# Optimization experiments

Measured on AMD Instinct MI355X. Metric: run time of the kernel, lower is better.

Reference implementation:

```python
import jax, jax.numpy as jnp
import numpy as np

K = 27          # kernel_size^3
N_IN = 150000   # active input sites
N_OUT = 150000  # active output sites
C_IN = 64
C_OUT = 64
R = 50000       # rules per kernel offset (equal counts -> vectorized grouped GEMM)


def setup_inputs() -> dict:
    key = jax.random.key(0)
    k1, k2, k3, k4 = jax.random.split(key, 4)
    # kaiming_normal_ fan_out, relu: std = sqrt(2 / fan_out) with fan_out = C_OUT
    w_std = float(np.sqrt(2.0 / C_OUT))
    return {
        "x_data": jax.random.normal(k1, (N_IN, C_IN), dtype=jnp.float32),
        "weights": jax.random.normal(k2, (K, C_IN, C_OUT), dtype=jnp.float32) * w_std,
        "bias": jnp.zeros((C_OUT,), dtype=jnp.float32),
        "in_idx": jax.random.randint(k3, (K * R,), 0, N_IN, dtype=jnp.int32),
        "out_idx": jax.random.randint(k4, (K * R,), 0, N_OUT, dtype=jnp.int32),
    }


def reference(x_data, weights, bias, in_idx, out_idx):
    # Rulebook sparse 3D conv: per-offset gather -> GEMM -> scatter-add.
    gathered = x_data[in_idx].reshape(K, R, C_IN)           # [K, R, Cin]
    vals = jnp.einsum('krc,kco->kro', gathered, weights)    # [K, R, Cout]
    out = jnp.zeros((N_OUT, C_OUT), dtype=x_data.dtype)
    out = out.at[out_idx].add(vals.reshape(K * R, C_OUT))   # atomic scatter-add
    return out + bias[None, :]
```

## Files before the change

kernel.cpp:

```cpp
#include <hip/hip_runtime.h>
#include <hip/hip_bf16.h>


typedef __bf16 bf16x8_t __attribute__((ext_vector_type(8)));
typedef __bf16 bf16x2_t __attribute__((ext_vector_type(2)));
typedef float f32x4_t __attribute__((ext_vector_type(4)));

#define KOFF 27
#define RULES 50000
#define KR (KOFF * RULES)
#define CIN 64
#define COUT 64
#define NIN 150000
#define NOUT 150000
#define BR 256
#define BPK ((RULES + BR - 1) / BR)

#define OFF_OFF 0ull
#define OFF_BSUM 600064ull
#define OFF_RANK 600832ull
#define OFF_XB 6000896ull
#define OFF_VALS_FULL 25200896ull
#define OFF_VALS_MID 6000896ull
#define WS_FULL (25200896ull + 172800000ull)
#define WS_MID (6000896ull + 172800000ull)

__device__ __forceinline__ void gload_lds16(const void* g, void* l) {
  __builtin_amdgcn_global_load_lds(
      (const __attribute__((address_space(1))) unsigned int*)g,
      (__attribute__((address_space(3))) unsigned int*)l, 16, 0, 0);
}

__global__ __launch_bounds__(256) void k_cvt(const float* __restrict__ x,
                                             __bf16* __restrict__ xb) {
  const int i = blockIdx.x * 256 + threadIdx.x;
  if (i < NIN * CIN / 8) {
    const float4 f0 = reinterpret_cast<const float4*>(x)[i * 2];
    const float4 f1 = reinterpret_cast<const float4*>(x)[i * 2 + 1];
    bf16x8_t v;
    v[0] = (__bf16)f0.x; v[1] = (__bf16)f0.y; v[2] = (__bf16)f0.z; v[3] = (__bf16)f0.w;
    v[4] = (__bf16)f1.x; v[5] = (__bf16)f1.y; v[6] = (__bf16)f1.z; v[7] = (__bf16)f1.w;
    reinterpret_cast<bf16x8_t*>(xb)[i] = v;
  }
}

__global__ __launch_bounds__(256) void k_zero(int* __restrict__ cnt) {
  const int i = blockIdx.x * 256 + threadIdx.x;
  if (i < NOUT) cnt[i] = 0;
}

__global__ __launch_bounds__(256) void k_count(const int* __restrict__ out_idx,
                                               int* __restrict__ cnt,
                                               int* __restrict__ rankl) {
  const int i = blockIdx.x * 256 + threadIdx.x;
  if (i < KR) rankl[i] = atomicAdd(&cnt[out_idx[i]], 1);
}

__global__ __launch_bounds__(1024) void k_scan1(int* __restrict__ off,
                                                int* __restrict__ bsum) {
  __shared__ int s[1024];
  const int t = threadIdx.x;
  const int i = blockIdx.x * 1024 + t;
  const int v = (i < NOUT) ? off[i] : 0;
  s[t] = v;
  __syncthreads();
#pragma unroll
  for (int d = 1; d < 1024; d <<= 1) {
    const int u = (t >= d) ? s[t - d] : 0;
    __syncthreads();
    s[t] += u;
    __syncthreads();
  }
  if (i < NOUT) off[i] = s[t] - v;
  if (t == 1023) bsum[blockIdx.x] = s[1023];
}

__global__ __launch_bounds__(256) void k_scan2(int* __restrict__ bsum, int nb) {
  __shared__ int s[256];
  const int t = threadIdx.x;
  const int v = (t < nb) ? bsum[t] : 0;
  s[t] = v;
  __syncthreads();
#pragma unroll
  for (int d = 1; d < 256; d <<= 1) {
    const int u = (t >= d) ? s[t - d] : 0;
    __syncthreads();
    s[t] += u;
    __syncthreads();
  }
  if (t < nb) bsum[t] = s[t] - v;
}

__global__ __launch_bounds__(256) void k_scan3(int* __restrict__ off,
                                               const int* __restrict__ bsum) {
  const int i = blockIdx.x * 256 + threadIdx.x;
  if (i < NOUT) off[i] += bsum[i >> 10];
  if (i == 0) off[NOUT] = KR;
}

__global__ __launch_bounds__(256) void pass1_bf16(
    const __bf16* __restrict__ xb, const float* __restrict__ w,
    const int* __restrict__ in_idx, const int* __restrict__ out_idx,
    const int* __restrict__ off_arr, const int* __restrict__ rankl,
    __bf16* __restrict__ vals) {
  __shared__ char lds[256 * 128 + 64 * 128];
  char* const Abase = lds;
  char* const Bbase = lds + 256 * 128;

  const int bid = blockIdx.x;
  const int k = bid / BPK;
  const int rblk = bid - k * BPK;
  const int rule0 = rblk * BR;
  const int t = threadIdx.x;
  const int wid = t >> 6;
  const int lane = t & 63;

  {
    const int rowInWave = lane >> 3;
    const int srcChunk = (lane & 7) ^ rowInWave;
    const int* idxBase = in_idx + (size_t)k * RULES;
#pragma unroll
    for (int it = 0; it < 8; ++it) {
      const int rbase = it * 32 + wid * 8;
      int rule = rule0 + rbase + rowInWave;
      if (rule > RULES - 1) rule = RULES - 1;
      const int src = idxBase[rule];
      const __bf16* gp = xb + ((size_t)src << 6) + (srcChunk << 3);
      gload_lds16(gp, Abase + rbase * 128 + lane * 16);
    }
  }

  {
    const int c = t >> 2;
    const int o0 = (t & 3) * 16;
    const float* wp = w + ((size_t)k * CIN + c) * COUT + o0;
#pragma unroll
    for (int j4 = 0; j4 < 4; ++j4) {
      const float4 f = *reinterpret_cast<const float4*>(wp + j4 * 4);
#pragma unroll
      for (int e = 0; e < 4; ++e) {
        const int o = o0 + j4 * 4 + e;
        const float val = (e == 0) ? f.x : (e == 1) ? f.y : (e == 2) ? f.z : f.w;
        const int addr = o * 128 + ((c * 2) ^ ((o & 7) << 4));
        *reinterpret_cast<__bf16*>(Bbase + addr) = (__bf16)val;
      }
    }
  }

  __syncthreads();

  const int rA = lane & 15;
  const int g = lane >> 4;

  bf16x8_t af[4][2];
  bf16x8_t bfr[4][2];
#pragma unroll
  for (int m = 0; m < 4; ++m)
#pragma unroll
    for (int kk = 0; kk < 2; ++kk) {
      const int r = wid * 64 + m * 16 + rA;
      const int colByte = (kk * 64 + g * 16) ^ ((r & 7) << 4);
      af[m][kk] = *reinterpret_cast<const bf16x8_t*>(Abase + r * 128 + colByte);
    }
#pragma unroll
  for (int n = 0; n < 4; ++n)
#pragma unroll
    for (int kk = 0; kk < 2; ++kk) {
      const int o = n * 16 + rA;
      const int colByte = (kk * 64 + g * 16) ^ ((o & 7) << 4);
      bfr[n][kk] = *reinterpret_cast<const bf16x8_t*>(Bbase + o * 128 + colByte);
    }

  __syncthreads();

  f32x4_t acc[4][4];
#pragma unroll
  for (int m = 0; m < 4; ++m)
#pragma unroll
    for (int n = 0; n < 4; ++n)
#pragma unroll
      for (int e = 0; e < 4; ++e) acc[m][n][e] = 0.0f;

#pragma unroll
  for (int kk = 0; kk < 2; ++kk)
#pragma unroll
    for (int m = 0; m < 4; ++m)
#pragma unroll
      for (int n = 0; n < 4; ++n)
        acc[m][n] = __builtin_amdgcn_mfma_f32_16x16x32_bf16(
            af[m][kk], bfr[n][kk], acc[m][n], 0, 0, 0);

  const bool evenLane = (rA & 1) == 0;
#pragma unroll
  for (int m = 0; m < 4; ++m) {
#pragma unroll
    for (int j = 0; j < 4; ++j) {
      const int rr = wid * 64 + m * 16 + g * 4 + j;
      float mine[4], other[4];
#pragma unroll
      for (int n = 0; n < 4; ++n) {
        mine[n] = acc[m][n][j];
        other[n] = __shfl_xor(mine[n], 1, 64);
      }
      const int swz = (rr & 7) << 4;
      if (evenLane) {
#pragma unroll
        for (int n = 0; n < 2; ++n) {
          bf16x2_t p; p[0] = (__bf16)mine[n]; p[1] = (__bf16)other[n];
          const int col = n * 16 + rA;
          *reinterpret_cast<bf16x2_t*>(Abase + rr * 128 + ((col * 2) ^ swz)) = p;
        }
      } else {
#pragma unroll
        for (int n = 2; n < 4; ++n) {
          bf16x2_t p; p[0] = (__bf16)other[n]; p[1] = (__bf16)mine[n];
          const int col = n * 16 + rA - 1;
          *reinterpret_cast<bf16x2_t*>(Abase + rr * 128 + ((col * 2) ^ swz)) = p;
        }
      }
    }
  }

  __syncthreads();

  {
    const int chunk = t & 7;
    const int r0 = t >> 3;
#pragma unroll
    for (int pass = 0; pass < 8; ++pass) {
      const int r = r0 + pass * 32;
      const int rule = rule0 + r;
      if (rule < RULES) {
        const size_t gi = (size_t)k * RULES + rule;
        const int dst = off_arr[out_idx[gi]] + rankl[gi];
        const bf16x8_t v = *reinterpret_cast<const bf16x8_t*>(
            Abase + r * 128 + ((chunk * 16) ^ ((r & 7) << 4)));
        *reinterpret_cast<bf16x8_t*>(vals + (size_t)dst * COUT + chunk * 8) = v;
      }
    }
  }
}

__global__ __launch_bounds__(256) void pass1_f32(
    const float* __restrict__ x, const float* __restrict__ w,
    const int* __restrict__ in_idx, const int* __restrict__ out_idx,
    const int* __restrict__ off_arr, const int* __restrict__ rankl,
    __bf16* __restrict__ vals) {
  __shared__ char lds[256 * 128 + 64 * 128];
  char* const Abase = lds;
  char* const Bbase = lds + 256 * 128;

  const int bid = blockIdx.x;
  const int k = bid / BPK;
  const int rblk = bid - k * BPK;
  const int rule0 = rblk * BR;
  const int t = threadIdx.x;

  {
    const int chunk = t & 7;
    const int r0 = t >> 3;
#pragma unroll
    for (int pass = 0; pass < 8; ++pass) {
      const int r = r0 + pass * 32;
      const int rule = rule0 + r;
      bf16x8_t v;
      if (rule < RULES) {
        const int src = in_idx[(size_t)k * RULES + rule];
        const float* p = x + (size_t)src * CIN + chunk * 8;
        const float4 f0 = *reinterpret_cast<const float4*>(p);
        const float4 f1 = *reinterpret_cast<const float4*>(p + 4);
        v[0] = (__bf16)f0.x; v[1] = (__bf16)f0.y;
        v[2] = (__bf16)f0.z; v[3] = (__bf16)f0.w;
        v[4] = (__bf16)f1.x; v[5] = (__bf16)f1.y;
        v[6] = (__bf16)f1.z; v[7] = (__bf16)f1.w;
      } else {
#pragma unroll
        for (int e = 0; e < 8; ++e) v[e] = (__bf16)0.0f;
      }
      const int colByte = (chunk * 16) ^ ((r & 7) << 4);
      *reinterpret_cast<bf16x8_t*>(Abase + r * 128 + colByte) = v;
    }
  }
  {
    const int c = t >> 2;
    const int o0 = (t & 3) * 16;
    const float* wp = w + ((size_t)k * CIN + c) * COUT + o0;
#pragma unroll
    for (int j4 = 0; j4 < 4; ++j4) {
      const float4 f = *reinterpret_cast<const float4*>(wp + j4 * 4);
#pragma unroll
      for (int e = 0; e < 4; ++e) {
        const int o = o0 + j4 * 4 + e;
        const float val = (e == 0) ? f.x : (e == 1) ? f.y : (e == 2) ? f.z : f.w;
        const int addr = o * 128 + ((c * 2) ^ ((o & 7) << 4));
        *reinterpret_cast<__bf16*>(Bbase + addr) = (__bf16)val;
      }
    }
  }
  __syncthreads();

  const int wid = t >> 6;
  const int l = t & 63;
  const int rA = l & 15;
  const int g = l >> 4;

  bf16x8_t af[4][2];
  bf16x8_t bfr[4][2];
#pragma unroll
  for (int m = 0; m < 4; ++m)
#pragma unroll
    for (int kk = 0; kk < 2; ++kk) {
      const int r = wid * 64 + m * 16 + rA;
      const int colByte = (kk * 64 + g * 16) ^ ((r & 7) << 4);
      af[m][kk] = *reinterpret_cast<const bf16x8_t*>(Abase + r * 128 + colByte);
    }
#pragma unroll
  for (int n = 0; n < 4; ++n)
#pragma unroll
    for (int kk = 0; kk < 2; ++kk) {
      const int o = n * 16 + rA;
      const int colByte = (kk * 64 + g * 16) ^ ((o & 7) << 4);
      bfr[n][kk] = *reinterpret_cast<const bf16x8_t*>(Bbase + o * 128 + colByte);
    }

  __syncthreads();

  f32x4_t acc[4][4];
#pragma unroll
  for (int m = 0; m < 4; ++m)
#pragma unroll
    for (int n = 0; n < 4; ++n)
#pragma unroll
      for (int e = 0; e < 4; ++e) acc[m][n][e] = 0.0f;

#pragma unroll
  for (int kk = 0; kk < 2; ++kk)
#pragma unroll
    for (int m = 0; m < 4; ++m)
#pragma unroll
      for (int n = 0; n < 4; ++n)
        acc[m][n] = __builtin_amdgcn_mfma_f32_16x16x32_bf16(
            af[m][kk], bfr[n][kk], acc[m][n], 0, 0, 0);

  const bool evenLane = (rA & 1) == 0;
#pragma unroll
  for (int m = 0; m < 4; ++m) {
#pragma unroll
    for (int j = 0; j < 4; ++j) {
      const int rr = wid * 64 + m * 16 + g * 4 + j;
      float mine[4], other[4];
#pragma unroll
      for (int n = 0; n < 4; ++n) {
        mine[n] = acc[m][n][j];
        other[n] = __shfl_xor(mine[n], 1, 64);
      }
      const int swz = (rr & 7) << 4;
      if (evenLane) {
#pragma unroll
        for (int n = 0; n < 2; ++n) {
          bf16x2_t p; p[0] = (__bf16)mine[n]; p[1] = (__bf16)other[n];
          const int col = n * 16 + rA;
          *reinterpret_cast<bf16x2_t*>(Abase + rr * 128 + ((col * 2) ^ swz)) = p;
        }
      } else {
#pragma unroll
        for (int n = 2; n < 4; ++n) {
          bf16x2_t p; p[0] = (__bf16)other[n]; p[1] = (__bf16)mine[n];
          const int col = n * 16 + rA - 1;
          *reinterpret_cast<bf16x2_t*>(Abase + rr * 128 + ((col * 2) ^ swz)) = p;
        }
      }
    }
  }

  __syncthreads();

  {
    const int chunk = t & 7;
    const int r0 = t >> 3;
#pragma unroll
    for (int pass = 0; pass < 8; ++pass) {
      const int r = r0 + pass * 32;
      const int rule = rule0 + r;
      if (rule < RULES) {
        const size_t gi = (size_t)k * RULES + rule;
        const int dst = off_arr[out_idx[gi]] + rankl[gi];
        const bf16x8_t v = *reinterpret_cast<const bf16x8_t*>(
            Abase + r * 128 + ((chunk * 16) ^ ((r & 7) << 4)));
        *reinterpret_cast<bf16x8_t*>(vals + (size_t)dst * COUT + chunk * 8) = v;
      }
    }
  }
}

__global__ __launch_bounds__(256) void pass2_kernel(
    const __bf16* __restrict__ vals, const int* __restrict__ off,
    const float* __restrict__ bias, float* __restrict__ out) {
  const int lane = threadIdx.x & 63;
  const int o = blockIdx.x * 4 + (threadIdx.x >> 6);
  if (o >= NOUT) return;

  float acc = bias[lane];
  const int r0 = off[o];
  const int r1 = off[o + 1];
  const __bf16* vp = vals + (size_t)r0 * COUT + lane;
  for (int j = r0; j < r1; ++j, vp += COUT) acc += (float)*vp;
  out[(size_t)o * COUT + lane] = acc;
}

__global__ __launch_bounds__(256) void init_out_kernel(
    const float* __restrict__ bias, float* __restrict__ out, int total4) {
  const int i = blockIdx.x * blockDim.x + threadIdx.x;
  if (i < total4) {
    const float4 v = reinterpret_cast<const float4*>(bias)[i & 15];
    reinterpret_cast<float4*>(out)[i] = v;
  }
}

__global__ __launch_bounds__(256) void spconv_atomic_kernel(
    const float* __restrict__ x, const float* __restrict__ w,
    const int* __restrict__ in_idx, const int* __restrict__ out_idx,
    float* __restrict__ out) {
  __shared__ char lds[256 * 128 + 64 * 128];
  char* const Abase = lds;
  char* const Bbase = lds + 256 * 128;

  const int bid = blockIdx.x;
  const int k = bid / BPK;
  const int rblk = bid - k * BPK;
  const int rule0 = rblk * BR;
  const int t = threadIdx.x;

  {
    const int chunk = t & 7;
    const int r0 = t >> 3;
#pragma unroll
    for (int pass = 0; pass < 8; ++pass) {
      const int r = r0 + pass * 32;
      const int rule = rule0 + r;
      bf16x8_t v;
      if (rule < RULES) {
        const int src = in_idx[(size_t)k * RULES + rule];
        const float* p = x + (size_t)src * CIN + chunk * 8;
        const float4 f0 = *reinterpret_cast<const float4*>(p);
        const float4 f1 = *reinterpret_cast<const float4*>(p + 4);
        v[0] = (__bf16)f0.x; v[1] = (__bf16)f0.y;
        v[2] = (__bf16)f0.z; v[3] = (__bf16)f0.w;
        v[4] = (__bf16)f1.x; v[5] = (__bf16)f1.y;
        v[6] = (__bf16)f1.z; v[7] = (__bf16)f1.w;
      } else {
#pragma unroll
        for (int e = 0; e < 8; ++e) v[e] = (__bf16)0.0f;
      }
      const int colByte = (chunk * 16) ^ ((r & 7) << 4);
      *reinterpret_cast<bf16x8_t*>(Abase + r * 128 + colByte) = v;
    }
  }
  {
    const int c = t >> 2;
    const int o0 = (t & 3) * 16;
    const float* wp = w + ((size_t)k * CIN + c) * COUT + o0;
#pragma unroll
    for (int j4 = 0; j4 < 4; ++j4) {
      const float4 f = *reinterpret_cast<const float4*>(wp + j4 * 4);
#pragma unroll
      for (int e = 0; e < 4; ++e) {
        const int o = o0 + j4 * 4 + e;
        const float val = (e == 0) ? f.x : (e == 1) ? f.y : (e == 2) ? f.z : f.w;
        const int addr = o * 128 + ((c * 2) ^ ((o & 7) << 4));
        *reinterpret_cast<__bf16*>(Bbase + addr) = (__bf16)val;
      }
    }
  }
  __syncthreads();

  const int wid = t >> 6;
  const int l = t & 63;
  const int rA = l & 15;
  const int g = l >> 4;

  bf16x8_t af[4][2];
  bf16x8_t bfr[4][2];
#pragma unroll
  for (int m = 0; m < 4; ++m)
#pragma unroll
    for (int kk = 0; kk < 2; ++kk) {
      const int r = wid * 64 + m * 16 + rA;
      const int colByte = (kk * 64 + g * 16) ^ ((r & 7) << 4);
      af[m][kk] = *reinterpret_cast<const bf16x8_t*>(Abase + r * 128 + colByte);
    }
#pragma unroll
  for (int n = 0; n < 4; ++n)
#pragma unroll
    for (int kk = 0; kk < 2; ++kk) {
      const int o = n * 16 + rA;
      const int colByte = (kk * 64 + g * 16) ^ ((o & 7) << 4);
      bfr[n][kk] = *reinterpret_cast<const bf16x8_t*>(Bbase + o * 128 + colByte);
    }

  f32x4_t acc[4][4];
#pragma unroll
  for (int m = 0; m < 4; ++m)
#pragma unroll
    for (int n = 0; n < 4; ++n)
#pragma unroll
      for (int e = 0; e < 4; ++e) acc[m][n][e] = 0.0f;

#pragma unroll
  for (int kk = 0; kk < 2; ++kk)
#pragma unroll
    for (int m = 0; m < 4; ++m)
#pragma unroll
      for (int n = 0; n < 4; ++n)
        acc[m][n] = __builtin_amdgcn_mfma_f32_16x16x32_bf16(
            af[m][kk], bfr[n][kk], acc[m][n], 0, 0, 0);

#pragma unroll
  for (int m = 0; m < 4; ++m)
#pragma unroll
    for (int j = 0; j < 4; ++j) {
      const int rr = wid * 64 + m * 16 + g * 4 + j;
      const int rule = rule0 + rr;
      if (rule < RULES) {
        const int orow = out_idx[(size_t)k * RULES + rule];
        float* op = out + (size_t)orow * COUT + rA;
#pragma unroll
        for (int n = 0; n < 4; ++n) atomicAdd(op + n * 16, acc[m][n][j]);
      }
    }
}

extern "C" void kernel_launch(void* const* d_in, const int* in_sizes, int n_in,
                              void* d_out, int out_size, void* d_ws, size_t ws_size,
                              hipStream_t stream) {
  const float* x = (const float*)d_in[0];
  const float* w = (const float*)d_in[1];
  const float* bias = (const float*)d_in[2];
  const int* in_idx = (const int*)d_in[3];
  const int* out_idx = (const int*)d_in[4];
  float* out = (float*)d_out;

  if (ws_size >= WS_MID) {
    char* ws = (char*)d_ws;
    int* off = (int*)(ws + OFF_OFF);
    int* bsum = (int*)(ws + OFF_BSUM);
    int* rankl = (int*)(ws + OFF_RANK);
    const bool full = (ws_size >= WS_FULL);
    __bf16* xb = (__bf16*)(ws + OFF_XB);
    __bf16* vals = (__bf16*)(ws + (full ? OFF_VALS_FULL : OFF_VALS_MID));

    const int nb1 = (NOUT + 1023) / 1024;
    if (full) k_cvt<<<(NIN * CIN / 8 + 255) / 256, 256, 0, stream>>>(x, xb);
    k_zero<<<(NOUT + 255) / 256, 256, 0, stream>>>(off);
    k_count<<<(KR + 255) / 256, 256, 0, stream>>>(out_idx, off, rankl);
    k_scan1<<<nb1, 1024, 0, stream>>>(off, bsum);
    k_scan2<<<1, 256, 0, stream>>>(bsum, nb1);
    k_scan3<<<(NOUT + 255) / 256, 256, 0, stream>>>(off, bsum);
    if (full) {
      pass1_bf16<<<KOFF * BPK, 256, 0, stream>>>(xb, w, in_idx, out_idx, off,
                                                 rankl, vals);
    } else {
      pass1_f32<<<KOFF * BPK, 256, 0, stream>>>(x, w, in_idx, out_idx, off,
                                                rankl, vals);
    }
    pass2_kernel<<<(NOUT + 3) / 4, 256, 0, stream>>>(vals, off, bias, out);
  } else {
    const int total4 = NOUT * COUT / 4;
    init_out_kernel<<<(total4 + 255) / 256, 256, 0, stream>>>(bias, out, total4);
    spconv_atomic_kernel<<<KOFF * BPK, 256, 0, stream>>>(x, w, in_idx, out_idx, out);
  }
}
```

Baseline: 325.9 us.

## Vectorize count kernel and rewrite segmented reduction with 16-byte loads and LDS atomics

k_count now has each thread read four out_idx values as one int4 and store four ranks in one int4. pass2 is restructured so each block handles 64 output rows: threads stream the block's contiguous range of CSR-sorted bf16 rows with 16-byte loads, find the owning row by binary search over offsets held in LDS, and accumulate with LDS float atomics. The block then writes coalesced float4 outputs with bias added. This replaces the old per-lane 2-byte strided loads, which made poor use of memory bandwidth, at the cost of LDS atomic contention and the binary-search overhead.

```diff
diff --git a/kernel.cpp b/kernel.cpp
--- a/kernel.cpp
+++ b/kernel.cpp
@@ -15,6 +15,7 @@
 #define NOUT 150000
 #define BR 256
 #define BPK ((RULES + BR - 1) / BR)
+#define P2ROWS 64
 
 #define OFF_OFF 0ull
 #define OFF_BSUM 600064ull
@@ -53,7 +54,15 @@
                                                int* __restrict__ cnt,
                                                int* __restrict__ rankl) {
   const int i = blockIdx.x * 256 + threadIdx.x;
-  if (i < KR) rankl[i] = atomicAdd(&cnt[out_idx[i]], 1);
+  if (i < KR / 4) {
+    const int4 v = reinterpret_cast<const int4*>(out_idx)[i];
+    int4 r;
+    r.x = atomicAdd(&cnt[v.x], 1);
+    r.y = atomicAdd(&cnt[v.y], 1);
+    r.z = atomicAdd(&cnt[v.z], 1);
+    r.w = atomicAdd(&cnt[v.w], 1);
+    reinterpret_cast<int4*>(rankl)[i] = r;
+  }
 }
 
 __global__ __launch_bounds__(1024) void k_scan1(int* __restrict__ off,
@@ -396,16 +405,58 @@
 __global__ __launch_bounds__(256) void pass2_kernel(
     const __bf16* __restrict__ vals, const int* __restrict__ off,
     const float* __restrict__ bias, float* __restrict__ out) {
-  const int lane = threadIdx.x & 63;
-  const int o = blockIdx.x * 4 + (threadIdx.x >> 6);
-  if (o >= NOUT) return;
-
-  float acc = bias[lane];
-  const int r0 = off[o];
-  const int r1 = off[o + 1];
-  const __bf16* vp = vals + (size_t)r0 * COUT + lane;
-  for (int j = r0; j < r1; ++j, vp += COUT) acc += (float)*vp;
-  out[(size_t)o * COUT + lane] = acc;
+  __shared__ int offs[P2ROWS + 1];
+  __shared__ float acc[P2ROWS][65];
+
+  const int t = threadIdx.x;
+  const int row0 = blockIdx.x * P2ROWS;
+
+  if (t <= P2ROWS) {
+    int r = row0 + t;
+    if (r > NOUT) r = NOUT;
+    offs[t] = off[r];
+  }
+  for (int i = t; i < P2ROWS * 65; i += 256)
+    (&acc[0][0])[i] = 0.0f;
+  __syncthreads();
+
+  const int S = offs[0];
+  const int E = offs[P2ROWS];
+  const int chunk = t & 7;
+  const int q = t >> 3;
+
+  for (int j = S + q; j < E; j += 32) {
+    const bf16x8_t v =
+        *reinterpret_cast<const bf16x8_t*>(vals + (size_t)j * COUT + chunk * 8);
+    int lo = 0, hi = P2ROWS;
+    while (hi - lo > 1) {
+      const int mid = (lo + hi) >> 1;
+      if (j >= offs[mid]) lo = mid; else hi = mid;
+    }
+#pragma unroll
+    for (int e = 0; e < 8; ++e)
+      atomicAdd(&acc[lo][chunk * 8 + e], (float)v[e]);
+  }
+
+  __syncthreads();
+
+  {
+    const int r = t >> 2;
+    const int c0 = (t & 3) * 16;
+    if (row0 + r < NOUT) {
+      float* op = out + (size_t)(row0 + r) * COUT + c0;
+#pragma unroll
+      for (int v4 = 0; v4 < 4; ++v4) {
+        const float4 b = reinterpret_cast<const float4*>(bias)[(c0 >> 2) + v4];
+        float4 o;
+        o.x = acc[r][c0 + v4 * 4 + 0] + b.x;
+        o.y = acc[r][c0 + v4 * 4 + 1] + b.y;
+        o.z = acc[r][c0 + v4 * 4 + 2] + b.z;
+        o.w = acc[r][c0 + v4 * 4 + 3] + b.w;
+        reinterpret_cast<float4*>(op)[v4] = o;
+      }
+    }
+  }
 }
 
 __global__ __launch_bounds__(256) void init_out_kernel(
@@ -552,7 +603,7 @@
     const int nb1 = (NOUT + 1023) / 1024;
     if (full) k_cvt<<<(NIN * CIN / 8 + 255) / 256, 256, 0, stream>>>(x, xb);
     k_zero<<<(NOUT + 255) / 256, 256, 0, stream>>>(off);
-    k_count<<<(KR + 255) / 256, 256, 0, stream>>>(out_idx, off, rankl);
+    k_count<<<(KR / 4 + 255) / 256, 256, 0, stream>>>(out_idx, off, rankl);
     k_scan1<<<nb1, 1024, 0, stream>>>(off, bsum);
     k_scan2<<<1, 256, 0, stream>>>(bsum, nb1);
     k_scan3<<<(NOUT + 255) / 256, 256, 0, stream>>>(off, bsum);
@@ -563,7 +614,8 @@
       pass1_f32<<<KOFF * BPK, 256, 0, stream>>>(x, w, in_idx, out_idx, off,
                                                 rankl, vals);
     }
-    pass2_kernel<<<(NOUT + 3) / 4, 256, 0, stream>>>(vals, off, bias, out);
+    pass2_kernel<<<(NOUT + P2ROWS - 1) / P2ROWS, 256, 0, stream>>>(vals, off,
+                                                                   bias, out);
   } else {
     const int total4 = NOUT * COUT / 4;
     init_out_kernel<<<(total4 + 255) / 256, 256, 0, stream>>>(bias, out, total4);
```

Result: slower. 730.9 us (+124.3%).
